# Kernel tuning notes

Measured on AMD Instinct MI355X. Metric: run time of the kernel, lower is better.

The kernel has to match this reference:

```python
import jax, jax.numpy as jnp
import numpy as np

K = 16  # buckets per block (2**treeDepth)
DEPTH = 4

_BIT_BASE = np.array([
 [-1,-1,0,-1,0,0,0,-1,0,0,0,0,0,0,0],[-1,-1,0,-1,0,0,0,1,0,0,0,0,0,0,0],
 [-1,-1,0,1,0,0,0,0,-1,0,0,0,0,0,0],[-1,-1,0,1,0,0,0,0,1,0,0,0,0,0,0],
 [-1,1,0,0,-1,0,0,0,0,-1,0,0,0,0,0],[-1,1,0,0,-1,0,0,0,0,1,0,0,0,0,0],
 [-1,1,0,0,1,0,0,0,0,0,-1,0,0,0,0],[-1,1,0,0,1,0,0,0,0,0,1,0,0,0,0],
 [1,0,-1,0,0,-1,0,0,0,0,0,-1,0,0,0],[1,0,-1,0,0,-1,0,0,0,0,0,1,0,0,0],
 [1,0,-1,0,0,1,0,0,0,0,0,0,-1,0,0],[1,0,-1,0,0,1,0,0,0,0,0,0,1,0,0],
 [1,0,1,0,0,0,-1,0,0,0,0,0,0,-1,0],[1,0,1,0,0,0,-1,0,0,0,0,0,0,1,0],
 [1,0,1,0,0,0,1,0,0,0,0,0,0,0,-1],[1,0,1,0,0,0,1,0,0,0,0,0,0,0,1]], dtype=np.float32)

def make_tree_des_matrix(C):
    # block-diagonal, but off-blocks are ONES per the original code (init with ones)
    m = np.ones((C * K, C * (K - 1)), dtype=np.float32)
    for c in range(C):
        m[c*K:(c+1)*K, c*(K-1):(c+1)*(K-1)] = _BIT_BASE
    return jnp.asarray(m)

def make_selection_matrix(C):
    base = np.zeros((K - 1, DEPTH), dtype=np.float32)
    base[0, 0] = 1.0
    for i in range(1, K - 1):
        base[i, int(np.log2(i + 1))] = 1.0
    sel = np.zeros((C * (K - 1), C * DEPTH), dtype=np.float32)
    for c in range(C):
        sel[c*(K-1):(c+1)*(K-1), c*DEPTH:(c+1)*DEPTH] = base
    return jnp.asarray(sel)

def setup_inputs() -> dict:
    key = jax.random.key(0)
    k1, k2, k3, k4 = jax.random.split(key, 4)
    N, D, C, M = 32768, 1024, 64, 1024
    inputMatrix = jax.random.normal(k1, (N, D), dtype=jnp.float32)
    dims = jax.random.randint(k2, (C * DEPTH,), 0, D)  # gather indices into input columns
    thresholds = jax.random.normal(k3, (C * (K - 1), 1), dtype=jnp.float32)
    lut = jax.random.normal(k4, (M, C, K), dtype=jnp.float32)
    return {
        "inputMatrix": inputMatrix,
        "dims": dims,
        "thresholds": thresholds,
        "lut": lut,
        "selection_matrix": make_selection_matrix(C),
        "tree_des_mat": make_tree_des_matrix(C),
    }

def reference(inputMatrix, dims, thresholds, lut, selection_matrix, tree_des_mat):
    N = inputMatrix.shape[0]
    M, C, Kb = lut.shape
    chosen = inputMatrix[:, dims]                              # [N, C*4]
    subtracted = selection_matrix @ chosen.T - thresholds      # [C*15, N]
    tanh_h = jnp.tanh(subtracted)
    sign_ste = jnp.sign(subtracted) - jax.lax.stop_gradient(tanh_h) + tanh_h
    tree = (tree_des_mat @ sign_ste).T.reshape(N, C, Kb)       # [N, C, 16]
    soft = jax.nn.softmax(tree, axis=2)
    hard = jax.nn.one_hot(jnp.argmax(soft, axis=2), Kb, dtype=soft.dtype)
    encoded = hard - jax.lax.stop_gradient(soft) + soft        # hard-forward / soft-backward STE
    # einsum('nij,kij->nki').sum(2) == full contraction over (C, K)
    out = jnp.einsum('nck,mck->nm', encoded, lut)              # [N, M]
    return out
```

## Files before the change

### kernel.cpp

```cpp
#include <hip/hip_runtime.h>
#include <stdint.h>

#define N_ROWS 32768
#define D_DIM  1024
#define C_TREES 64
#define K_LEAF 16
#define M_OUT  1024

typedef _Float16 half8v __attribute__((ext_vector_type(8)));
typedef _Float16 half4v __attribute__((ext_vector_type(4)));

__global__ __launch_bounds__(256) void k_transpose(const float* __restrict__ lut,
                                                   float* __restrict__ lutT) {
    __shared__ float tile[32][33];
    int bx = blockIdx.x;
    int by = blockIdx.y;
    int tx = threadIdx.x;
    int ty = threadIdx.y;
    int src_col = bx * 32 + tx;
#pragma unroll
    for (int i = 0; i < 4; ++i) {
        int src_row = by * 32 + ty + i * 8;
        tile[ty + i * 8][tx] = lut[(size_t)src_row * 1024 + src_col];
    }
    __syncthreads();
    int dst_col = by * 32 + tx;
#pragma unroll
    for (int i = 0; i < 4; ++i) {
        int dst_row = bx * 32 + ty + i * 8;
        lutT[(size_t)dst_row * 1024 + dst_col] = tile[tx][ty + i * 8];
    }
}

__global__ __launch_bounds__(256) void k_build_h(const float* __restrict__ lutT,
                                                 _Float16* __restrict__ Ph) {
    int j = blockIdx.x;
    int p = blockIdx.y;
    int klo = j & 15;
    int khi = j >> 4;
    int t = threadIdx.x;
    const float4* a = (const float4*)lutT + (size_t)(p * 32 + klo) * 256;
    const float4* b = (const float4*)lutT + (size_t)(p * 32 + 16 + khi) * 256;
    float4 va = a[t];
    float4 vb = b[t];
    half4v hv;
    hv.x = (_Float16)(va.x + vb.x);
    hv.y = (_Float16)(va.y + vb.y);
    hv.z = (_Float16)(va.z + vb.z);
    hv.w = (_Float16)(va.w + vb.w);
    ((half4v*)Ph)[(size_t)(p * 256 + j) * 256 + t] = hv;
}

__global__ __launch_bounds__(256) void k_encode2(const float* __restrict__ in,
                                                 const int* __restrict__ dims,
                                                 const float* __restrict__ th,
                                                 uint8_t* __restrict__ code) {
    __shared__ float rows[8][1028];
    __shared__ float th_s[960];
    __shared__ int   dims_s[256];
    int t = threadIdx.x;
    dims_s[t] = dims[t];
    for (int i = t; i < 960; i += 256) th_s[i] = th[i];
    int n0 = blockIdx.x * 8;
    const float4* in4 = (const float4*)(in + (size_t)n0 * 1024);
#pragma unroll
    for (int i = 0; i < 8; ++i) {
        ((float4*)&rows[i][0])[t] = in4[i * 256 + t];
    }
    __syncthreads();
    int p = t >> 3;
    int r = t & 7;
    const float* trow = &rows[r][0];
    int cA = 2 * p, cB = 2 * p + 1;

    float xA[4], xB[4];
#pragma unroll
    for (int l = 0; l < 4; ++l) {
        xA[l] = trow[dims_s[cA * 4 + l]];
        xB[l] = trow[dims_s[cB * 4 + l]];
    }
    const float* tAp = &th_s[cA * 15];
    const float* tBp = &th_s[cB * 15];
    unsigned mA = 0, mB = 0;
#pragma unroll
    for (int i = 0; i < 15; ++i) {
        const int d = (i == 0) ? 0 : (i < 3) ? 1 : (i < 7) ? 2 : 3;
        mA |= ((unsigned)(xA[d] > tAp[i])) << i;
        mB |= ((unsigned)(xB[d] > tBp[i])) << i;
    }
    int nA = 0, nB = 0;
#pragma unroll
    for (int l = 0; l < 4; ++l) {
        nA = 2 * nA + 1 + ((mA >> nA) & 1);
        nB = 2 * nB + 1 + ((mB >> nB) & 1);
    }
    code[(size_t)p * N_ROWS + n0 + r] = (uint8_t)(((nB - 15) << 4) | (nA - 15));
}

__global__ __launch_bounds__(512, 4) void k_accum4(const float4* __restrict__ P4h,
                                                   const uint8_t* __restrict__ code,
                                                   float* __restrict__ out) {
    __shared__ float4 sl[2][2048];

    int t  = threadIdx.x;
    int mc = t & 7;
    int ng = t >> 3;
    int m0 = blockIdx.x * 64;
    int n0 = blockIdx.y * 512;

    auto stage = [&](int buf, int p) {
#pragma unroll
        for (int it = 0; it < 4; ++it) {
            int idx = t + it * 512;
            int row = idx >> 3;
            int ch  = idx & 7;
            const float4* src = P4h + ((size_t)(p * 256 + row)) * 128 + (m0 >> 3) + ch;
            __builtin_amdgcn_global_load_lds((const __attribute__((address_space(1))) void*)src,
                                             (__attribute__((address_space(3))) void*)(&sl[buf][idx]),
                                             16, 0, 0);
        }
    };

    float acc[8][8];
#pragma unroll
    for (int j = 0; j < 8; ++j)
#pragma unroll
        for (int q = 0; q < 8; ++q) acc[j][q] = 0.f;

    const uint8_t* cp = code + n0 + ng * 8;
    uint64_t cd = *(const uint64_t*)cp;
    stage(0, 0);

    for (int p = 0; p < 32; ++p) {
        __syncthreads();
        if (p < 31) stage((p + 1) & 1, p + 1);
        uint64_t nx = 0;
        if (p < 31) nx = *(const uint64_t*)(cp + (size_t)(p + 1) * N_ROWS);
        const float4* s = &sl[p & 1][0];
#pragma unroll
        for (int j = 0; j < 8; ++j) {
            int cv = (int)((cd >> (8 * j)) & 0xff);
            float4 v = s[cv * 8 + mc];
            half8v h = __builtin_bit_cast(half8v, v);
#pragma unroll
            for (int q = 0; q < 8; ++q) acc[j][q] += (float)h[q];
        }
        cd = nx;
    }

    float4* out4 = (float4*)out;
#pragma unroll
    for (int j = 0; j < 8; ++j) {
        int n = n0 + ng * 8 + j;
        size_t base = (size_t)n * 256 + (m0 >> 2) + mc * 2;
        out4[base]     = make_float4(acc[j][0], acc[j][1], acc[j][2], acc[j][3]);
        out4[base + 1] = make_float4(acc[j][4], acc[j][5], acc[j][6], acc[j][7]);
    }
}

__global__ __launch_bounds__(256) void k_encode(const float* __restrict__ in,
                                                const int* __restrict__ dims,
                                                const float* __restrict__ th,
                                                uint8_t* __restrict__ leaf) {
    __shared__ float rows[8][1028];
    __shared__ float th_s[960];
    __shared__ int   dims_s[256];
    int t = threadIdx.x;
    dims_s[t] = dims[t];
    for (int i = t; i < 960; i += 256) th_s[i] = th[i];
    int n0 = blockIdx.x * 8;
    const float4* in4 = (const float4*)(in + (size_t)n0 * 1024);
#pragma unroll
    for (int i = 0; i < 8; ++i) {
        ((float4*)&rows[i][0])[t] = in4[i * 256 + t];
    }
    __syncthreads();
#pragma unroll
    for (int i = 0; i < 2; ++i) {
        int id = i * 256 + t;
        int c = id >> 3;
        int r = id & 7;
        int node = 0;
        const float* trow = &rows[r][0];
#pragma unroll
        for (int lvl = 0; lvl < 4; ++lvl) {
            float x   = trow[dims_s[c * 4 + lvl]];
            float thv = th_s[c * 15 + node];
            node = 2 * node + 1 + ((x > thv) ? 1 : 0);
        }
        leaf[(size_t)c * N_ROWS + n0 + r] = (uint8_t)(node - 15);
    }
}

__global__ __launch_bounds__(512) void k_accum(const float* __restrict__ lutT,
                                               const uint8_t* __restrict__ leaf,
                                               float* __restrict__ out) {
    __shared__ float4 sl[2][16][32];
    int t     = threadIdx.x;
    int mlane = t & 31;
    int ngrp  = t >> 5;
    int wave  = t >> 6;
    int lane  = t & 63;
    int srow  = 2 * wave + (lane >> 5);
    int schunk = lane & 31;
    int m0 = blockIdx.x * 128;
    int n0 = blockIdx.y * 128;
    const float4* lutT4 = (const float4*)lutT;
    auto stage = [&](int buf, int c) {
        const float4* src = lutT4 + ((size_t)(c * 16 + srow) * 256) + (m0 >> 2) + schunk;
        __builtin_amdgcn_global_load_lds((const __attribute__((address_space(1))) void*)src,
                                         (__attribute__((address_space(3))) void*)&sl[buf][2 * wave][0],
                                         16, 0, 0);
    };
    float4 acc[8];
#pragma unroll
    for (int j = 0; j < 8; ++j) acc[j] = make_float4(0.f, 0.f, 0.f, 0.f);
    const uint8_t* lp = leaf + n0 + ngrp * 8;
    uint64_t lv = *(const uint64_t*)lp;
    stage(0, 0);
#pragma unroll 2
    for (int c = 0; c < 64; ++c) {
        __syncthreads();
        if (c < 63) stage((c + 1) & 1, c + 1);
        uint64_t lv_next = (c < 63) ? *(const uint64_t*)(lp + (size_t)(c + 1) * N_ROWS) : 0ull;
        int buf = c & 1;
#pragma unroll
        for (int j = 0; j < 8; ++j) {
            int k = (int)((lv >> (8 * j)) & 15);
            float4 v = sl[buf][k][mlane];
            acc[j].x += v.x; acc[j].y += v.y; acc[j].z += v.z; acc[j].w += v.w;
        }
        lv = lv_next;
    }
    float4* out4 = (float4*)out;
#pragma unroll
    for (int j = 0; j < 8; ++j) {
        int n = n0 + ngrp * 8 + j;
        out4[(size_t)n * 256 + (m0 >> 2) + mlane] = acc[j];
    }
}

extern "C" void kernel_launch(void* const* d_in, const int* in_sizes, int n_in,
                              void* d_out, int out_size, void* d_ws, size_t ws_size,
                              hipStream_t stream) {
    const float* inputMatrix = (const float*)d_in[0];
    const int*   dims        = (const int*)d_in[1];
    const float* thresholds  = (const float*)d_in[2];
    const float* lut         = (const float*)d_in[3];
    float* out = (float*)d_out;

    float* lutT = (float*)d_ws;

    const size_t NEED = (size_t)4 * 1024 * 1024
                      + (size_t)16 * 1024 * 1024
                      + (size_t)1 * 1024 * 1024;

    if (ws_size >= NEED) {
        _Float16* Ph   = (_Float16*)((char*)d_ws + (size_t)4 * 1024 * 1024);
        uint8_t* codep = (uint8_t*)d_ws + (size_t)20 * 1024 * 1024;

        k_transpose<<<dim3(32, 32), dim3(32, 8), 0, stream>>>(lut, lutT);
        k_build_h<<<dim3(256, 32), 256, 0, stream>>>(lutT, Ph);
        k_encode2<<<N_ROWS / 8, 256, 0, stream>>>(inputMatrix, dims, thresholds, codep);
        k_accum4<<<dim3(M_OUT / 64, N_ROWS / 512), 512, 0, stream>>>((const float4*)Ph, codep, out);
    } else {
        uint8_t* leaf = (uint8_t*)d_ws + (size_t)4 * 1024 * 1024;
        k_transpose<<<dim3(32, 32), dim3(32, 8), 0, stream>>>(lut, lutT);
        k_encode<<<N_ROWS / 8, 256, 0, stream>>>(inputMatrix, dims, thresholds, leaf);
        k_accum<<<dim3(M_OUT / 128, N_ROWS / 128), 512, 0, stream>>>(lutT, leaf, out);
    }
}
```

Measured before the change: 332.3 us.

## Retile accumulation kernel with 4-stage LDS pipeline and fma_mix accumulation

Replaces k_accum4 with k_accum5. The new kernel covers 32 output columns by 1024 rows per block instead of 64 by 512, and uses four quarter-size LDS buffers loaded three stages ahead. It also swaps __syncthreads for manual s_waitcnt vmcnt plus s_barrier, and does the half-to-float accumulation with inline v_fma_mix_f32 instead of separate convert and add. The aim is to hide global-to-LDS load latency and cut ALU instructions in the inner loop. The cost is heavier reliance on hand-counted vmcnt values that must match the issued load order, and an output tile that is twice as narrow in M.

```diff
diff --git a/kernel.cpp b/kernel.cpp
--- a/kernel.cpp
+++ b/kernel.cpp
@@ -97,24 +97,25 @@
     code[(size_t)p * N_ROWS + n0 + r] = (uint8_t)(((nB - 15) << 4) | (nA - 15));
 }
 
-__global__ __launch_bounds__(512, 4) void k_accum4(const float4* __restrict__ P4h,
+__global__ __launch_bounds__(512, 4) void k_accum5(const float4* __restrict__ P4h,
                                                    const uint8_t* __restrict__ code,
                                                    float* __restrict__ out) {
-    __shared__ float4 sl[2][2048];
+    __shared__ float4 sl[4][1024];
 
     int t  = threadIdx.x;
-    int mc = t & 7;
-    int ng = t >> 3;
-    int m0 = blockIdx.x * 64;
-    int n0 = blockIdx.y * 512;
+    int mc = t & 3;
+    int ng = t >> 2;
+    int m0 = blockIdx.x * 32;
+    int n0 = blockIdx.y * 1024;
+    const int mch0 = m0 >> 3;
 
     auto stage = [&](int buf, int p) {
 #pragma unroll
-        for (int it = 0; it < 4; ++it) {
+        for (int it = 0; it < 2; ++it) {
             int idx = t + it * 512;
-            int row = idx >> 3;
-            int ch  = idx & 7;
-            const float4* src = P4h + ((size_t)(p * 256 + row)) * 128 + (m0 >> 3) + ch;
+            int row = idx >> 2;
+            int ch  = idx & 3;
+            const float4* src = P4h + ((size_t)(p * 256 + row)) * 128 + mch0 + ch;
             __builtin_amdgcn_global_load_lds((const __attribute__((address_space(1))) void*)src,
                                              (__attribute__((address_space(3))) void*)(&sl[buf][idx]),
                                              16, 0, 0);
@@ -128,25 +129,45 @@
         for (int q = 0; q < 8; ++q) acc[j][q] = 0.f;
 
     const uint8_t* cp = code + n0 + ng * 8;
+
     uint64_t cd = *(const uint64_t*)cp;
+    asm volatile("" ::: "memory");
     stage(0, 0);
-
-    for (int p = 0; p < 32; ++p) {
-        __syncthreads();
-        if (p < 31) stage((p + 1) & 1, p + 1);
-        uint64_t nx = 0;
-        if (p < 31) nx = *(const uint64_t*)(cp + (size_t)(p + 1) * N_ROWS);
-        const float4* s = &sl[p & 1][0];
-#pragma unroll
-        for (int j = 0; j < 8; ++j) {
-            int cv = (int)((cd >> (8 * j)) & 0xff);
-            float4 v = s[cv * 8 + mc];
-            half8v h = __builtin_bit_cast(half8v, v);
-#pragma unroll
-            for (int q = 0; q < 8; ++q) acc[j][q] += (float)h[q];
-        }
-        cd = nx;
-    }
+    stage(1, 1);
+    stage(2, 2);
+
+#define ACC_ITER(P_, WAIT_)                                                          \
+    do {                                                                             \
+        asm volatile("s_waitcnt vmcnt(" WAIT_ ")" ::: "memory");                     \
+        asm volatile("s_barrier" ::: "memory");                                      \
+        uint64_t nx = 0;                                                             \
+        if ((P_) < 31) nx = *(const uint64_t*)(cp + (size_t)((P_) + 1) * N_ROWS);    \
+        asm volatile("" ::: "memory");               \
+        if ((P_) + 3 < 32) stage(((P_) + 3) & 3, (P_) + 3);                          \
+        const float4* s = &sl[(P_) & 3][0];                                          \
+        _Pragma("unroll")                                                            \
+        for (int j = 0; j < 8; ++j) {                                                \
+            int cv = (int)((cd >> (8 * j)) & 0xff);                                  \
+            float4 v = s[cv * 4 + mc];                                               \
+            asm("v_fma_mix_f32 %0, %8, 1.0, %0 op_sel_hi:[1,0,0]\n\t"                \
+                "v_fma_mix_f32 %1, %8, 1.0, %1 op_sel:[1,0,0] op_sel_hi:[1,0,0]\n\t" \
+                "v_fma_mix_f32 %2, %9, 1.0, %2 op_sel_hi:[1,0,0]\n\t"                \
+                "v_fma_mix_f32 %3, %9, 1.0, %3 op_sel:[1,0,0] op_sel_hi:[1,0,0]\n\t" \
+                "v_fma_mix_f32 %4, %10, 1.0, %4 op_sel_hi:[1,0,0]\n\t"               \
+                "v_fma_mix_f32 %5, %10, 1.0, %5 op_sel:[1,0,0] op_sel_hi:[1,0,0]\n\t"\
+                "v_fma_mix_f32 %6, %11, 1.0, %6 op_sel_hi:[1,0,0]\n\t"               \
+                "v_fma_mix_f32 %7, %11, 1.0, %7 op_sel:[1,0,0] op_sel_hi:[1,0,0]"    \
+                : "+v"(acc[j][0]), "+v"(acc[j][1]), "+v"(acc[j][2]), "+v"(acc[j][3]),\
+                  "+v"(acc[j][4]), "+v"(acc[j][5]), "+v"(acc[j][6]), "+v"(acc[j][7]) \
+                : "v"(v.x), "v"(v.y), "v"(v.z), "v"(v.w));                           \
+        }                                                                            \
+        cd = nx;                                                                     \
+    } while (0)
+
+    for (int p = 0; p < 30; ++p) ACC_ITER(p, "4");
+    ACC_ITER(30, "3");
+    ACC_ITER(31, "1");
+#undef ACC_ITER
 
     float4* out4 = (float4*)out;
 #pragma unroll
@@ -262,7 +283,7 @@
         k_transpose<<<dim3(32, 32), dim3(32, 8), 0, stream>>>(lut, lutT);
         k_build_h<<<dim3(256, 32), 256, 0, stream>>>(lutT, Ph);
         k_encode2<<<N_ROWS / 8, 256, 0, stream>>>(inputMatrix, dims, thresholds, codep);
-        k_accum4<<<dim3(M_OUT / 64, N_ROWS / 512), 512, 0, stream>>>((const float4*)Ph, codep, out);
+        k_accum5<<<dim3(M_OUT / 32, N_ROWS / 1024), 512, 0, stream>>>((const float4*)Ph, codep, out);
     } else {
         uint8_t* leaf = (uint8_t*)d_ws + (size_t)4 * 1024 * 1024;
         k_transpose<<<dim3(32, 32), dim3(32, 8), 0, stream>>>(lut, lutT);
```

New measurement: 318.5 us. -4.1%, faster.

## Tile paired LUT by M-columns, split slices between LDS and direct global gathers

Applied to the files above, without the earlier changes.

The paired fp16 LUT is stored tile-major so each block loads contiguous 32-column slices. The accumulation kernel now handles 32 output columns per block with 4 rows per thread and a triple-buffered LDS pipeline. Even tree-pair slices are read from LDS, while odd slices are gathered straight from global/L2, which halves LDS staging traffic. Accumulation uses inline v_fma_mix_f32 to add fp16 values into fp32 without separate conversions. Waits and barriers are issued by hand via inline asm, which is fragile if the compiler reorders the loads.

```diff
diff --git a/kernel.cpp b/kernel.cpp
--- a/kernel.cpp
+++ b/kernel.cpp
@@ -9,6 +9,20 @@
 
 typedef _Float16 half8v __attribute__((ext_vector_type(8)));
 typedef _Float16 half4v __attribute__((ext_vector_type(4)));
+
+__device__ __forceinline__ void fma8(float* a, float4 v) {
+    asm("v_fma_mix_f32 %0, %8, 1.0, %0 op_sel_hi:[1,0,0]\n\t"
+        "v_fma_mix_f32 %1, %8, 1.0, %1 op_sel:[1,0,0] op_sel_hi:[1,0,0]\n\t"
+        "v_fma_mix_f32 %2, %9, 1.0, %2 op_sel_hi:[1,0,0]\n\t"
+        "v_fma_mix_f32 %3, %9, 1.0, %3 op_sel:[1,0,0] op_sel_hi:[1,0,0]\n\t"
+        "v_fma_mix_f32 %4, %10, 1.0, %4 op_sel_hi:[1,0,0]\n\t"
+        "v_fma_mix_f32 %5, %10, 1.0, %5 op_sel:[1,0,0] op_sel_hi:[1,0,0]\n\t"
+        "v_fma_mix_f32 %6, %11, 1.0, %6 op_sel_hi:[1,0,0]\n\t"
+        "v_fma_mix_f32 %7, %11, 1.0, %7 op_sel:[1,0,0] op_sel_hi:[1,0,0]"
+        : "+v"(a[0]), "+v"(a[1]), "+v"(a[2]), "+v"(a[3]),
+          "+v"(a[4]), "+v"(a[5]), "+v"(a[6]), "+v"(a[7])
+        : "v"(v.x), "v"(v.y), "v"(v.z), "v"(v.w));
+}
 
 __global__ __launch_bounds__(256) void k_transpose(const float* __restrict__ lut,
                                                    float* __restrict__ lutT) {
@@ -32,8 +46,8 @@
     }
 }
 
-__global__ __launch_bounds__(256) void k_build_h(const float* __restrict__ lutT,
-                                                 _Float16* __restrict__ Ph) {
+__global__ __launch_bounds__(256) void k_build_ht(const float* __restrict__ lutT,
+                                                  _Float16* __restrict__ Pt) {
     int j = blockIdx.x;
     int p = blockIdx.y;
     int klo = j & 15;
@@ -48,7 +62,8 @@
     hv.y = (_Float16)(va.y + vb.y);
     hv.z = (_Float16)(va.z + vb.z);
     hv.w = (_Float16)(va.w + vb.w);
-    ((half4v*)Ph)[(size_t)(p * 256 + j) * 256 + t] = hv;
+    int tile = t >> 3;
+    ((half4v*)Pt)[(size_t)tile * 65536 + (size_t)(p * 256 + j) * 8 + (t & 7)] = hv;
 }
 
 __global__ __launch_bounds__(256) void k_encode2(const float* __restrict__ in,
@@ -97,62 +112,89 @@
     code[(size_t)p * N_ROWS + n0 + r] = (uint8_t)(((nB - 15) << 4) | (nA - 15));
 }
 
-__global__ __launch_bounds__(512, 4) void k_accum4(const float4* __restrict__ P4h,
+__global__ __launch_bounds__(512, 6) void k_accum6(const _Float16* __restrict__ Pt,
                                                    const uint8_t* __restrict__ code,
                                                    float* __restrict__ out) {
-    __shared__ float4 sl[2][2048];
+    __shared__ float4 sl[3][1024];
 
     int t  = threadIdx.x;
-    int mc = t & 7;
-    int ng = t >> 3;
-    int m0 = blockIdx.x * 64;
+    int mc = t & 3;
+    int ng = t >> 2;
+    int tile = blockIdx.x;
     int n0 = blockIdx.y * 512;
-
-    auto stage = [&](int buf, int p) {
-#pragma unroll
-        for (int it = 0; it < 4; ++it) {
+    const float4* Pt4 = (const float4*)Pt + (size_t)tile * 32768;
+
+    auto stage = [&](int buf, int slice) {
+#pragma unroll
+        for (int it = 0; it < 2; ++it) {
             int idx = t + it * 512;
-            int row = idx >> 3;
-            int ch  = idx & 7;
-            const float4* src = P4h + ((size_t)(p * 256 + row)) * 128 + (m0 >> 3) + ch;
+            const float4* src = Pt4 + slice * 1024 + idx;
             __builtin_amdgcn_global_load_lds((const __attribute__((address_space(1))) void*)src,
                                              (__attribute__((address_space(3))) void*)(&sl[buf][idx]),
                                              16, 0, 0);
         }
     };
 
-    float acc[8][8];
-#pragma unroll
-    for (int j = 0; j < 8; ++j)
+    float acc[4][8];
+#pragma unroll
+    for (int j = 0; j < 4; ++j)
 #pragma unroll
         for (int q = 0; q < 8; ++q) acc[j][q] = 0.f;
 
-    const uint8_t* cp = code + n0 + ng * 8;
-    uint64_t cd = *(const uint64_t*)cp;
+    const uint8_t* cp = code + n0 + ng * 4;
+    uint32_t cdE = *(const uint32_t*)cp;
+    uint32_t cdO = *(const uint32_t*)(cp + N_ROWS);
+    asm volatile("" ::: "memory");
     stage(0, 0);
-
-    for (int p = 0; p < 32; ++p) {
-        __syncthreads();
-        if (p < 31) stage((p + 1) & 1, p + 1);
-        uint64_t nx = 0;
-        if (p < 31) nx = *(const uint64_t*)(cp + (size_t)(p + 1) * N_ROWS);
-        const float4* s = &sl[p & 1][0];
-#pragma unroll
-        for (int j = 0; j < 8; ++j) {
-            int cv = (int)((cd >> (8 * j)) & 0xff);
-            float4 v = s[cv * 8 + mc];
-            half8v h = __builtin_bit_cast(half8v, v);
-#pragma unroll
-            for (int q = 0; q < 8; ++q) acc[j][q] += (float)h[q];
-        }
-        cd = nx;
+    stage(1, 2);
+    int bc = 0;
+
+    for (int i = 0; i < 16; ++i) {
+        asm volatile("s_waitcnt vmcnt(4)" ::: "memory");
+        asm volatile("s_barrier" ::: "memory");
+
+        int o = 2 * i + 1;
+        float4 gv0, gv1, gv2, gv3;
+        {
+            int c0 = (int)(cdO & 0xff);
+            int c1 = (int)((cdO >> 8) & 0xff);
+            int c2 = (int)((cdO >> 16) & 0xff);
+            int c3 = (int)((cdO >> 24) & 0xff);
+            int ob = o << 8;
+            gv0 = Pt4[(ob + c0) * 4 + mc];
+            gv1 = Pt4[(ob + c1) * 4 + mc];
+            gv2 = Pt4[(ob + c2) * 4 + mc];
+            gv3 = Pt4[(ob + c3) * 4 + mc];
+        }
+        int ip = (i < 15) ? (i + 1) : 0;
+        uint32_t cdE2 = *(const uint32_t*)(cp + (size_t)(2 * ip) * N_ROWS);
+        uint32_t cdO2 = *(const uint32_t*)(cp + (size_t)(2 * ip + 1) * N_ROWS);
+        asm volatile("" ::: "memory");
+        int ns = (i < 14) ? (2 * i + 4) : 0;
+        int bs = bc + 2; if (bs >= 3) bs -= 3;
+        stage(bs, ns);
+
+        const float4* s = &sl[bc][0];
+#pragma unroll
+        for (int j = 0; j < 4; ++j) {
+            int cv = (int)((cdE >> (8 * j)) & 0xff);
+            float4 v = s[cv * 4 + mc];
+            fma8(acc[j], v);
+        }
+        fma8(acc[0], gv0);
+        fma8(acc[1], gv1);
+        fma8(acc[2], gv2);
+        fma8(acc[3], gv3);
+
+        cdE = cdE2; cdO = cdO2;
+        bc = (bc == 2) ? 0 : bc + 1;
     }
 
     float4* out4 = (float4*)out;
 #pragma unroll
-    for (int j = 0; j < 8; ++j) {
-        int n = n0 + ng * 8 + j;
-        size_t base = (size_t)n * 256 + (m0 >> 2) + mc * 2;
+    for (int j = 0; j < 4; ++j) {
+        int n = n0 + ng * 4 + j;
+        size_t base = (size_t)n * 256 + tile * 8 + mc * 2;
         out4[base]     = make_float4(acc[j][0], acc[j][1], acc[j][2], acc[j][3]);
         out4[base + 1] = make_float4(acc[j][4], acc[j][5], acc[j][6], acc[j][7]);
     }
@@ -256,13 +298,13 @@
                       + (size_t)1 * 1024 * 1024;
 
     if (ws_size >= NEED) {
-        _Float16* Ph   = (_Float16*)((char*)d_ws + (size_t)4 * 1024 * 1024);
+        _Float16* Pt   = (_Float16*)((char*)d_ws + (size_t)4 * 1024 * 1024);
         uint8_t* codep = (uint8_t*)d_ws + (size_t)20 * 1024 * 1024;
 
         k_transpose<<<dim3(32, 32), dim3(32, 8), 0, stream>>>(lut, lutT);
-        k_build_h<<<dim3(256, 32), 256, 0, stream>>>(lutT, Ph);
+        k_build_ht<<<dim3(256, 32), 256, 0, stream>>>(lutT, Pt);
         k_encode2<<<N_ROWS / 8, 256, 0, stream>>>(inputMatrix, dims, thresholds, codep);
-        k_accum4<<<dim3(M_OUT / 64, N_ROWS / 512), 512, 0, stream>>>((const float4*)Ph, codep, out);
+        k_accum6<<<dim3(M_OUT / 32, N_ROWS / 512), 512, 0, stream>>>(Pt, codep, out);
     } else {
         uint8_t* leaf = (uint8_t*)d_ws + (size_t)4 * 1024 * 1024;
         k_transpose<<<dim3(32, 32), dim3(32, 8), 0, stream>>>(lut, lutT);
```

Result: faster. 310.8 us (-6.5%).
